# Optimization experiments

Measured on AMD Instinct MI355X. Metric: run time of the kernel, lower is better.

The kernel has to match this reference:

```python
import jax, jax.numpy as jnp
import numpy as np

NUM_HEADS = 16

def setup_inputs() -> dict:
    key = jax.random.key(0)
    k1, k2, k3 = jax.random.split(key, 3)
    B, N, C = 4, 4096, 1024
    x = jax.random.normal(k1, (B, N, C), dtype=jnp.float32)
    # xavier-uniform-ish scaled init for the dense kernels
    w_qkv = jax.random.normal(k2, (C, 3 * C), dtype=jnp.float32) * (2.0 / (C + 3 * C)) ** 0.5
    w_proj = jax.random.normal(k3, (C, C), dtype=jnp.float32) * (1.0 / C) ** 0.5
    b_proj = jnp.zeros((C,), dtype=jnp.float32)
    return {"x": x, "w_qkv": w_qkv, "w_proj": w_proj, "b_proj": b_proj}

def reference(x, w_qkv, w_proj, b_proj):
    B, N, C = x.shape
    H = NUM_HEADS
    D = C // H
    # qkv projection: (B, N, 3C) -> (3, B, H, N, D)
    qkv = (x @ w_qkv).reshape(B, N, 3, H, D).transpose(2, 0, 3, 1, 4)
    q, k, v = qkv[0], qkv[1], qkv[2]
    # feature map: elu + 1 (positive features)
    q = jax.nn.elu(q) + 1.0
    k = jax.nn.elu(k) + 1.0
    # kv outer-product accumulation: (B, H, D, D)
    kv = jnp.einsum('bhnd,bhne->bhde', k, v)
    numerator = jnp.einsum('bhnd,bhde->bhne', q, kv)        # (B, H, N, D)
    sum_k = k.sum(axis=-2)                                   # (B, H, D)
    denominator = jnp.einsum('bhnd,bhd->bhn', q, sum_k)[..., None]  # (B, H, N, 1)
    y = numerator / denominator                              # (B, H, N, D)
    y = y.transpose(0, 2, 1, 3).reshape(B, N, C)             # merge heads
    out = y @ w_proj + b_proj
    return out
```

## Files before the change

### kernel.cpp

```cpp
#include <hip/hip_runtime.h>

typedef __bf16 bf16x8 __attribute__((ext_vector_type(8)));
typedef float f32x4 __attribute__((ext_vector_type(4)));

typedef const unsigned int __attribute__((address_space(1)))* gas_p;
typedef unsigned int __attribute__((address_space(3)))* las_p;

__device__ __forceinline__ void gload_lds16(const void* g, void* l) {
  __builtin_amdgcn_global_load_lds((gas_p)g, (las_p)l, 16, 0, 0);
}

__device__ __forceinline__ unsigned short f2bf(float f) {
  union { float f; unsigned int u; } x; x.f = f;
  unsigned int r = x.u + 0x7fffu + ((x.u >> 16) & 1u);
  return (unsigned short)(r >> 16);
}
__device__ __forceinline__ float elu1(float x) {
  return x > 0.f ? x + 1.f : __expf(x);
}
__device__ __forceinline__ f32x4 mfma16(bf16x8 a, bf16x8 b, f32x4 c) {
  return __builtin_amdgcn_mfma_f32_16x16x32_bf16(a, b, c, 0, 0, 0);
}

#define BAR() __builtin_amdgcn_s_barrier()
#define VMW4() asm volatile("s_waitcnt vmcnt(4)" ::: "memory")


__global__ __launch_bounds__(256) void k_cvt_x(const float* __restrict__ x,
                                               unsigned short* __restrict__ xb, int n) {
  int i = (blockIdx.x * 256 + threadIdx.x) * 4;
  const int stride = gridDim.x * 256 * 4;
  for (; i < n; i += stride) {
    float4 v = *(const float4*)(x + i);
    union { unsigned short u[4]; uint2 q; } pk;
    pk.u[0] = f2bf(v.x); pk.u[1] = f2bf(v.y); pk.u[2] = f2bf(v.z); pk.u[3] = f2bf(v.w);
    *(uint2*)(xb + i) = pk.q;
  }
}

__global__ __launch_bounds__(256) void k_cvt_t(const float* __restrict__ w,
                                               unsigned short* __restrict__ wT,
                                               int R, int Cc) {
  __shared__ float t[32][33];
  const int j0 = blockIdx.x * 32, i0 = blockIdx.y * 32;
  const int tx = threadIdx.x & 31, ty = threadIdx.x >> 5;
#pragma unroll
  for (int k = 0; k < 4; ++k)
    t[ty + 8 * k][tx] = w[(size_t)(i0 + ty + 8 * k) * Cc + j0 + tx];
  __syncthreads();
#pragma unroll
  for (int k = 0; k < 4; ++k)
    wT[(size_t)(j0 + ty + 8 * k) * R + i0 + tx] = f2bf(t[tx][ty + 8 * k]);
}


template <int EPI>
__global__ __launch_bounds__(512, 2) void k_gemm256(
    const unsigned short* __restrict__ A, const unsigned short* __restrict__ BT, int NBX,
    unsigned short* __restrict__ qb, unsigned short* __restrict__ kT,
    unsigned short* __restrict__ vT, const float* __restrict__ bias,
    float* __restrict__ out) {
  extern __shared__ unsigned short lds[];
  unsigned short* Asb = lds;
  unsigned short* Bsb = lds + 32768;

  const int tid = threadIdx.x, lane = tid & 63, wave = tid >> 6;
  const int wm = wave >> 2, wn = wave & 3;
  int bid = blockIdx.x;
  { const int cpx = (int)gridDim.x >> 3; bid = (bid & 7) * cpx + (bid >> 3); }
  const int bx = bid % NBX, by = bid / NBX;
  const size_t bm0 = (size_t)by << 8, bn0 = (size_t)bx << 8;

  const int srow = (wave << 4) + (lane >> 2);
  const int gscol = ((lane & 3) << 3) ^ (((srow >> 1) & 3) << 3);
  const unsigned short* Ag0 = A + (bm0 + srow) * 1024 + gscol;
  const unsigned short* Bg0 = BT + (bn0 + srow) * 1024 + gscol;
  unsigned short* Al0 = Asb + (wave << 9);
  unsigned short* Bl0 = Bsb + (wave << 9);

#define STAGE_A(OBH, KT)                                          \
  do {                                                            \
    const unsigned short* g_ = Ag0 + ((KT) << 6) + (OBH_K);       \
    unsigned short* l_ = Al0 + (OBH);                             \
    gload_lds16(g_, l_);                                          \
    gload_lds16(g_ + 128 * 1024, l_ + 4096);                      \
  } while (0)
#define STAGE_B(OBH, KT)                                          \
  do {                                                            \
    const unsigned short* g_ = Bg0 + ((KT) << 6) + (OBH_K);       \
    unsigned short* l_ = Bl0 + (OBH);                             \
    gload_lds16(g_, l_);                                          \
    gload_lds16(g_ + 128 * 1024, l_ + 4096);                      \
  } while (0)

  const int q8 = (((lane >> 4) << 3)) ^ (((lane >> 1) & 3) << 3);
  const int ar_base = (wm << 7) + (lane & 15);
  const int br_base = (wn << 6) + (lane & 15);

  f32x4 acc[8][4] = {};

  {
#define OBH_K 0
    STAGE_A(0, 0);
    STAGE_B(0, 0);
#undef OBH_K
#define OBH_K 32
    STAGE_A(8192, 0);
    STAGE_B(8192, 0);
#undef OBH_K
  }
  VMW4();
  BAR();

  for (int kt = 0; kt < 16; ++kt) {
    const int ob = (kt & 1) << 14;
    const int obn = ob ^ 16384;
    const int ktn = (kt < 15) ? kt + 1 : 15;
    bf16x8 af[4], bfr[4];

#pragma unroll
    for (int mi = 0; mi < 4; ++mi)
      af[mi] = *(const bf16x8*)&Asb[ob + ((ar_base + mi * 16) << 5) + q8];
#pragma unroll
    for (int n = 0; n < 4; ++n)
      bfr[n] = *(const bf16x8*)&Bsb[ob + ((br_base + n * 16) << 5) + q8];
#define OBH_K 0
    STAGE_A(obn, ktn);
#undef OBH_K
    BAR();
    __builtin_amdgcn_s_setprio(1);
#pragma unroll
    for (int mi = 0; mi < 4; ++mi)
#pragma unroll
      for (int n = 0; n < 4; ++n) acc[mi][n] = mfma16(af[mi], bfr[n], acc[mi][n]);
    __builtin_amdgcn_s_setprio(0);
    BAR();

#pragma unroll
    for (int mi = 0; mi < 4; ++mi)
      af[mi] = *(const bf16x8*)&Asb[ob + ((ar_base + 64 + mi * 16) << 5) + q8];
#define OBH_K 0
    STAGE_B(obn, ktn);
#undef OBH_K
    BAR();
    __builtin_amdgcn_s_setprio(1);
#pragma unroll
    for (int mi = 0; mi < 4; ++mi)
#pragma unroll
      for (int n = 0; n < 4; ++n) acc[4 + mi][n] = mfma16(af[mi], bfr[n], acc[4 + mi][n]);
    __builtin_amdgcn_s_setprio(0);
    VMW4();
    BAR();

#pragma unroll
    for (int mi = 0; mi < 4; ++mi)
      af[mi] = *(const bf16x8*)&Asb[ob + 8192 + ((ar_base + mi * 16) << 5) + q8];
#pragma unroll
    for (int n = 0; n < 4; ++n)
      bfr[n] = *(const bf16x8*)&Bsb[ob + 8192 + ((br_base + n * 16) << 5) + q8];
#define OBH_K 32
    STAGE_A(obn + 8192, ktn);
#undef OBH_K
    BAR();
    __builtin_amdgcn_s_setprio(1);
#pragma unroll
    for (int mi = 0; mi < 4; ++mi)
#pragma unroll
      for (int n = 0; n < 4; ++n) acc[mi][n] = mfma16(af[mi], bfr[n], acc[mi][n]);
    __builtin_amdgcn_s_setprio(0);
    BAR();

#pragma unroll
    for (int mi = 0; mi < 4; ++mi)
      af[mi] = *(const bf16x8*)&Asb[ob + 8192 + ((ar_base + 64 + mi * 16) << 5) + q8];
#define OBH_K 32
    STAGE_B(obn + 8192, ktn);
#undef OBH_K
    BAR();
    __builtin_amdgcn_s_setprio(1);
#pragma unroll
    for (int mi = 0; mi < 4; ++mi)
#pragma unroll
      for (int n = 0; n < 4; ++n) acc[4 + mi][n] = mfma16(af[mi], bfr[n], acc[4 + mi][n]);
    __builtin_amdgcn_s_setprio(0);
    VMW4();
    BAR();
  }

  const int rbase = (int)bm0 + (wm << 7) + ((lane >> 4) << 2);
  const int cbase = (int)bn0 + (wn << 6) + (lane & 15);
  if constexpr (EPI == 0) {
    const int reg3 = (int)(bn0 >> 10);
#pragma unroll
    for (int m = 0; m < 8; ++m) {
      const int rb = rbase + m * 16;
#pragma unroll
      for (int n = 0; n < 4; ++n) {
        const int col = cbase + n * 16;
        if (reg3 == 0) {
#pragma unroll
          for (int i = 0; i < 4; ++i)
            qb[(size_t)(rb + i) * 1024 + col] = f2bf(elu1(acc[m][n][i]));
        } else {
          const int jc = col & 1023, h = jc >> 6, d = jc & 63;
          const int b_ = rb >> 12, n_ = rb & 4095;
          union { unsigned short u[4]; uint2 q; } pk;
          if (reg3 == 1) {
#pragma unroll
            for (int i = 0; i < 4; ++i) pk.u[i] = f2bf(elu1(acc[m][n][i]));
          } else {
#pragma unroll
            for (int i = 0; i < 4; ++i) pk.u[i] = f2bf(acc[m][n][i]);
          }
          unsigned short* dst = (reg3 == 1) ? kT : vT;
          *(uint2*)(dst + ((size_t)((b_ * 16 + h) * 64 + d) * 4096 + n_)) = pk.q;
        }
      }
    }
  } else {
#pragma unroll
    for (int n = 0; n < 4; ++n) {
      const int col = cbase + n * 16;
      const float bc = bias[col];
#pragma unroll
      for (int m = 0; m < 8; ++m) {
        const int rb = rbase + m * 16;
#pragma unroll
        for (int i = 0; i < 4; ++i)
          out[(size_t)(rb + i) * 1024 + col] = acc[m][n][i] + bc;
      }
    }
  }
#undef STAGE_A
#undef STAGE_B
}


__global__ __launch_bounds__(256) void k_kvpart(const unsigned short* __restrict__ kT,
                                                const unsigned short* __restrict__ vT,
                                                float* __restrict__ kvp,
                                                float* __restrict__ sumkp) {
  __shared__ unsigned short Ks[64 * 64];
  __shared__ unsigned short Vs[64 * 64];
  const int blk = blockIdx.x;
  const int bh = blk >> 3, ch = blk & 7;
  const int tid = threadIdx.x, lane = tid & 63, wave = tid >> 6;
  const unsigned short* kb = kT + (size_t)bh * 64 * 4096;
  const unsigned short* vb = vT + (size_t)bh * 64 * 4096;
  const int n0 = ch * 512;
  const int lrow = lane >> 3;
  const int lcolz = (((lane & 7) ^ (lane >> 3)) << 3);
  f32x4 acc[5] = {};

  bf16x8 ones_frag;
  {
    unsigned short o = ((lane & 15) == 0) ? (unsigned short)0x3F80 : (unsigned short)0;
    union { unsigned short u[8]; bf16x8 v; } c;
#pragma unroll
    for (int i = 0; i < 8; ++i) c.u[i] = o;
    ones_frag = c.v;
  }

  const int rxor = (lane & 7) << 3;
  const int col0 = (((lane >> 4) << 3)) ^ rxor;
  const int col1 = ((32 + ((lane >> 4) << 3))) ^ rxor;

  for (int ks = 0; ks < 512; ks += 64) {
    __syncthreads();
#pragma unroll
    for (int i = 0; i < 2; ++i) {
      const int c = i * 4 + wave;
      gload_lds16(kb + (size_t)(c * 8 + lrow) * 4096 + n0 + ks + lcolz, &Ks[c * 512]);
      gload_lds16(vb + (size_t)(c * 8 + lrow) * 4096 + n0 + ks + lcolz, &Vs[c * 512]);
    }
    __syncthreads();
    const int ar = wave * 16 + (lane & 15);
#pragma unroll
    for (int kk = 0; kk < 2; ++kk) {
      const int co = kk ? col1 : col0;
      bf16x8 a = *(const bf16x8*)&Ks[ar * 64 + co];
#pragma unroll
      for (int n = 0; n < 4; ++n) {
        bf16x8 bv = *(const bf16x8*)&Vs[(n * 16 + (lane & 15)) * 64 + co];
        acc[n] = mfma16(a, bv, acc[n]);
      }
      acc[4] = mfma16(a, ones_frag, acc[4]);
    }
  }
  float* dst = kvp + (size_t)blk * 64 * 64;
  const int d0 = wave * 16 + ((lane >> 4) << 2);
#pragma unroll
  for (int n = 0; n < 4; ++n)
#pragma unroll
    for (int i = 0; i < 4; ++i)
      dst[(d0 + i) * 64 + n * 16 + (lane & 15)] = acc[n][i];
  if ((lane & 15) == 0) {
#pragma unroll
    for (int i = 0; i < 4; ++i) sumkp[(size_t)blk * 64 + d0 + i] = acc[4][i];
  }
}


__global__ __launch_bounds__(256) void k_kvred(const float* __restrict__ kvp,
                                               const float* __restrict__ sumkp,
                                               unsigned short* __restrict__ kvsk) {
  const int bh = blockIdx.x, tid = threadIdx.x;
  const float* src = kvp + (size_t)bh * 8 * 4096;
  unsigned short* dst = kvsk + (size_t)bh * 80 * 64;
#pragma unroll
  for (int it = 0; it < 16; ++it) {
    const int idx = tid + it * 256;
    const int e = idx >> 6, d = idx & 63;
    float s = 0.f;
#pragma unroll
    for (int c = 0; c < 8; ++c) s += src[c * 4096 + d * 64 + e];
    dst[idx] = f2bf(s);
  }
#pragma unroll
  for (int it = 0; it < 4; ++it) {
    const int idx = tid + it * 256;
    const int e2 = idx >> 6, d = idx & 63;
    float v = 0.f;
    if (e2 == 0) {
#pragma unroll
      for (int c = 0; c < 8; ++c) v += sumkp[(size_t)(bh * 8 + c) * 64 + d];
    }
    dst[64 * 64 + idx] = f2bf(v);
  }
}


__global__ __launch_bounds__(256) void k_numer(const unsigned short* __restrict__ qb,
                                               const unsigned short* __restrict__ kvsk,
                                               unsigned short* __restrict__ yb) {
  __shared__ unsigned short Bs[80 * 64];
  const int bh = blockIdx.y;
  const int b = bh >> 4, h = bh & 15;
  const int n0 = blockIdx.x << 7;
  const int tid = threadIdx.x, lane = tid & 63, wave = tid >> 6;
  {
    const uint4* src = (const uint4*)(kvsk + (size_t)bh * 80 * 64);
    uint4* dst = (uint4*)Bs;
    for (int i = tid; i < 640; i += 256) dst[i ^ ((i >> 3) & 7)] = src[i];
  }
  __syncthreads();

  const int ko = (lane >> 4) << 3;
  const int rx = (lane & 7) << 3;
  f32x4 acc[2][5] = {};
  const unsigned short* qrow =
      qb + (size_t)(b * 4096 + n0 + wave * 32 + (lane & 15)) * 1024 + h * 64;
#pragma unroll
  for (int kk = 0; kk < 2; ++kk) {
    bf16x8 a[2], bb[5];
#pragma unroll
    for (int m = 0; m < 2; ++m)
      a[m] = *(const bf16x8*)(qrow + (size_t)m * 16 * 1024 + ko + kk * 32);
#pragma unroll
    for (int n = 0; n < 5; ++n)
      bb[n] = *(const bf16x8*)&Bs[(n * 16 + (lane & 15)) * 64 + ((ko + kk * 32) ^ rx)];
#pragma unroll
    for (int m = 0; m < 2; ++m)
#pragma unroll
      for (int n = 0; n < 5; ++n)
        acc[m][n] = mfma16(a[m], bb[n], acc[m][n]);
  }

  const int rbase = b * 4096 + n0 + wave * 32 + ((lane >> 4) << 2);
#pragma unroll
  for (int m = 0; m < 2; ++m) {
    f32x4 inv;
#pragma unroll
    for (int i = 0; i < 4; ++i) {
      float den = __shfl(acc[m][4][i], lane & 48);
      inv[i] = __builtin_amdgcn_rcpf(den);
    }
#pragma unroll
    for (int n = 0; n < 4; ++n) {
      const int col = h * 64 + n * 16 + (lane & 15);
#pragma unroll
      for (int i = 0; i < 4; ++i)
        yb[(size_t)(rbase + m * 16 + i) * 1024 + col] = f2bf(acc[m][n][i] * inv[i]);
    }
  }
}


extern "C" void kernel_launch(void* const* d_in, const int* in_sizes, int n_in,
                              void* d_out, int out_size, void* d_ws, size_t ws_size,
                              hipStream_t stream) {
  const float* x = (const float*)d_in[0];
  const float* w_qkv = (const float*)d_in[1];
  const float* w_proj = (const float*)d_in[2];
  const float* b_proj = (const float*)d_in[3];
  float* out = (float*)d_out;
  char* ws = (char*)d_ws;

  unsigned short* xb = (unsigned short*)(ws);
  unsigned short* wqkvT = (unsigned short*)(ws + 33554432);
  unsigned short* wprojT = (unsigned short*)(ws + 39845888);
  unsigned short* qb = (unsigned short*)(ws + 41943040);
  unsigned short* kT = (unsigned short*)(ws + 75497472);
  unsigned short* vT = (unsigned short*)(ws + 109051904);
  float* kvp = (float*)(ws + 142606336);
  unsigned short* kvsk = (unsigned short*)(ws + 151011328);
  unsigned short* yb = xb;
  float* sumkp = (float*)wqkvT;

  k_cvt_x<<<2048, 256, 0, stream>>>(x, xb, 4 * 4096 * 1024);
  k_cvt_t<<<dim3(96, 32), 256, 0, stream>>>(w_qkv, wqkvT, 1024, 3072);
  k_cvt_t<<<dim3(32, 32), 256, 0, stream>>>(w_proj, wprojT, 1024, 1024);
  k_gemm256<0><<<768, 512, 131072, stream>>>(xb, wqkvT, 12, qb, kT, vT, nullptr, nullptr);
  k_kvpart<<<512, 256, 0, stream>>>(kT, vT, kvp, sumkp);
  k_kvred<<<64, 256, 0, stream>>>(kvp, sumkp, kvsk);
  k_numer<<<dim3(32, 64), 256, 0, stream>>>(qb, kvsk, yb);
  k_gemm256<1><<<256, 512, 131072, stream>>>(yb, wprojT, 4, nullptr, nullptr, nullptr,
                                             b_proj, out);
}
```

Measured before the change: 222.8 us.

## Deepen GEMM LDS pipeline to four half-tile slots with wider prefetch distance

The GEMM main loop changes from a two-buffer scheme to a four-slot ring of 32-wide K half-tiles. The prologue preloads three slots, and waits become vmcnt(8), so global-to-LDS loads run further ahead of the MFMA consumption. The loop is also fully unrolled, and the stage macros are replaced with lambdas. The aim is to hide global memory latency better, at the cost of more outstanding loads and a larger unrolled code size.

After: 221.2 us. About the same (-0.7%).

```diff
diff --git a/kernel.cpp b/kernel.cpp
--- a/kernel.cpp
+++ b/kernel.cpp
@@ -23,7 +23,9 @@
 }
 
 #define BAR() __builtin_amdgcn_s_barrier()
+#define VMW8() asm volatile("s_waitcnt vmcnt(8)" ::: "memory")
 #define VMW4() asm volatile("s_waitcnt vmcnt(4)" ::: "memory")
+#define VMW0() asm volatile("s_waitcnt vmcnt(0)" ::: "memory")
 
 
 __global__ __launch_bounds__(256) void k_cvt_x(const float* __restrict__ x,
@@ -75,58 +77,47 @@
   const int gscol = ((lane & 3) << 3) ^ (((srow >> 1) & 3) << 3);
   const unsigned short* Ag0 = A + (bm0 + srow) * 1024 + gscol;
   const unsigned short* Bg0 = BT + (bn0 + srow) * 1024 + gscol;
-  unsigned short* Al0 = Asb + (wave << 9);
-  unsigned short* Bl0 = Bsb + (wave << 9);
-
-#define STAGE_A(OBH, KT)                                          \
-  do {                                                            \
-    const unsigned short* g_ = Ag0 + ((KT) << 6) + (OBH_K);       \
-    unsigned short* l_ = Al0 + (OBH);                             \
-    gload_lds16(g_, l_);                                          \
-    gload_lds16(g_ + 128 * 1024, l_ + 4096);                      \
-  } while (0)
-#define STAGE_B(OBH, KT)                                          \
-  do {                                                            \
-    const unsigned short* g_ = Bg0 + ((KT) << 6) + (OBH_K);       \
-    unsigned short* l_ = Bl0 + (OBH);                             \
-    gload_lds16(g_, l_);                                          \
-    gload_lds16(g_ + 128 * 1024, l_ + 4096);                      \
-  } while (0)
-
-  const int q8 = (((lane >> 4) << 3)) ^ (((lane >> 1) & 3) << 3);
+  const int lws = wave << 9;
+
+  auto stageA = [&](int slot, int kt, int kh) {
+    const unsigned short* g_ = Ag0 + (kt << 6) + (kh << 5);
+    unsigned short* l_ = Asb + (slot << 13) + lws;
+    gload_lds16(g_, l_);
+    gload_lds16(g_ + 128 * 1024, l_ + 4096);
+  };
+  auto stageB = [&](int slot, int kt, int kh) {
+    const unsigned short* g_ = Bg0 + (kt << 6) + (kh << 5);
+    unsigned short* l_ = Bsb + (slot << 13) + lws;
+    gload_lds16(g_, l_);
+    gload_lds16(g_ + 128 * 1024, l_ + 4096);
+  };
+
+  const int q8 = ((lane >> 4) << 3) ^ (((lane >> 1) & 3) << 3);
   const int ar_base = (wm << 7) + (lane & 15);
   const int br_base = (wn << 6) + (lane & 15);
 
   f32x4 acc[8][4] = {};
 
-  {
-#define OBH_K 0
-    STAGE_A(0, 0);
-    STAGE_B(0, 0);
-#undef OBH_K
-#define OBH_K 32
-    STAGE_A(8192, 0);
-    STAGE_B(8192, 0);
-#undef OBH_K
-  }
-  VMW4();
+  stageA(0, 0, 0); stageB(0, 0, 0);
+  stageA(1, 0, 1); stageB(1, 0, 1);
+  stageA(2, 1, 0); stageB(2, 1, 0);
+  VMW8();
   BAR();
 
-  for (int kt = 0; kt < 16; ++kt) {
-    const int ob = (kt & 1) << 14;
-    const int obn = ob ^ 16384;
-    const int ktn = (kt < 15) ? kt + 1 : 15;
+#pragma unroll
+  for (int t = 0; t < 16; ++t) {
+    const int s0 = (2 * t) & 3, s1 = (2 * t + 1) & 3;
+    const int sA = (2 * t + 3) & 3, sB = (2 * t + 4) & 3;
+    const int t1 = t + 1, t2 = (t + 2 > 15) ? 15 : t + 2;
     bf16x8 af[4], bfr[4];
 
 #pragma unroll
     for (int mi = 0; mi < 4; ++mi)
-      af[mi] = *(const bf16x8*)&Asb[ob + ((ar_base + mi * 16) << 5) + q8];
+      af[mi] = *(const bf16x8*)&Asb[(s0 << 13) + ((ar_base + mi * 16) << 5) + q8];
 #pragma unroll
     for (int n = 0; n < 4; ++n)
-      bfr[n] = *(const bf16x8*)&Bsb[ob + ((br_base + n * 16) << 5) + q8];
-#define OBH_K 0
-    STAGE_A(obn, ktn);
-#undef OBH_K
+      bfr[n] = *(const bf16x8*)&Bsb[(s0 << 13) + ((br_base + n * 16) << 5) + q8];
+    if (t < 15) stageA(sA, t1, 1);
     BAR();
     __builtin_amdgcn_s_setprio(1);
 #pragma unroll
@@ -138,10 +129,8 @@
 
 #pragma unroll
     for (int mi = 0; mi < 4; ++mi)
-      af[mi] = *(const bf16x8*)&Asb[ob + ((ar_base + 64 + mi * 16) << 5) + q8];
-#define OBH_K 0
-    STAGE_B(obn, ktn);
-#undef OBH_K
+      af[mi] = *(const bf16x8*)&Asb[(s0 << 13) + ((ar_base + 64 + mi * 16) << 5) + q8];
+    if (t < 15) stageB(sA, t1, 1);
     BAR();
     __builtin_amdgcn_s_setprio(1);
 #pragma unroll
@@ -149,18 +138,16 @@
 #pragma unroll
       for (int n = 0; n < 4; ++n) acc[4 + mi][n] = mfma16(af[mi], bfr[n], acc[4 + mi][n]);
     __builtin_amdgcn_s_setprio(0);
-    VMW4();
-    BAR();
-
-#pragma unroll
-    for (int mi = 0; mi < 4; ++mi)
-      af[mi] = *(const bf16x8*)&Asb[ob + 8192 + ((ar_base + mi * 16) << 5) + q8];
+    if (t < 15) { VMW8(); } else { VMW4(); }
+    BAR();
+
+#pragma unroll
+    for (int mi = 0; mi < 4; ++mi)
+      af[mi] = *(const bf16x8*)&Asb[(s1 << 13) + ((ar_base + mi * 16) << 5) + q8];
 #pragma unroll
     for (int n = 0; n < 4; ++n)
-      bfr[n] = *(const bf16x8*)&Bsb[ob + 8192 + ((br_base + n * 16) << 5) + q8];
-#define OBH_K 32
-    STAGE_A(obn + 8192, ktn);
-#undef OBH_K
+      bfr[n] = *(const bf16x8*)&Bsb[(s1 << 13) + ((br_base + n * 16) << 5) + q8];
+    if (t < 15) stageA(sB, t2, 0);
     BAR();
     __builtin_amdgcn_s_setprio(1);
 #pragma unroll
@@ -172,10 +159,8 @@
 
 #pragma unroll
     for (int mi = 0; mi < 4; ++mi)
-      af[mi] = *(const bf16x8*)&Asb[ob + 8192 + ((ar_base + 64 + mi * 16) << 5) + q8];
-#define OBH_K 32
-    STAGE_B(obn + 8192, ktn);
-#undef OBH_K
+      af[mi] = *(const bf16x8*)&Asb[(s1 << 13) + ((ar_base + 64 + mi * 16) << 5) + q8];
+    if (t < 15) stageB(sB, t2, 0);
     BAR();
     __builtin_amdgcn_s_setprio(1);
 #pragma unroll
@@ -183,9 +168,10 @@
 #pragma unroll
       for (int n = 0; n < 4; ++n) acc[4 + mi][n] = mfma16(af[mi], bfr[n], acc[4 + mi][n]);
     __builtin_amdgcn_s_setprio(0);
-    VMW4();
-    BAR();
-  }
+    if (t < 15) VMW8();
+    BAR();
+  }
+  VMW0();
 
   const int rbase = (int)bm0 + (wm << 7) + ((lane >> 4) << 2);
   const int cbase = (int)bn0 + (wn << 6) + (lane & 15);
@@ -231,8 +217,6 @@
       }
     }
   }
-#undef STAGE_A
-#undef STAGE_B
 }
 
 
```
